# Performance work log

Hardware: AMD Instinct MI355X
Metric: run time of the kernel (lower is better)

## Reference

```python
import jax, jax.numpy as jnp
import numpy as np

B, T, S = 16, 512, 512
V, E, H = 10000, 512, 1024
L, K, MAXLEN = 6, 3, 1024
PAD_VAL = 1.0  # torch code pads conv input with tgt_pad_idx as a float value


def setup_inputs() -> dict:
    key = jax.random.key(0)
    ks = jax.random.split(key, 12)
    g = lambda k, shape: (jax.random.normal(k, shape, jnp.float32) * 0.02)
    return {
        "tgt": jax.random.randint(ks[0], (B, T), 0, V),
        "encoder_conved": jax.random.normal(ks[1], (B, S, E), jnp.float32),
        "encoder_combined": jax.random.normal(ks[2], (B, S, E), jnp.float32),
        "tok_emb": g(ks[3], (V, E)),
        "pos_emb": g(ks[4], (MAXLEN, E)),
        "emb2hid_w": g(ks[5], (E, H)), "emb2hid_b": jnp.zeros((H,), jnp.float32),
        "hid2emb_w": g(ks[6], (H, E)), "hid2emb_b": jnp.zeros((E,), jnp.float32),
        "attn_hid2emb_w": g(ks[7], (H, E)), "attn_hid2emb_b": jnp.zeros((E,), jnp.float32),
        "attn_emb2hid_w": g(ks[8], (E, H)), "attn_emb2hid_b": jnp.zeros((H,), jnp.float32),
        "fc_out_w": g(ks[9], (E, V)), "fc_out_b": jnp.zeros((V,), jnp.float32),
        "conv_w": g(ks[10], (L, 2 * H, H, K)),  # torch Conv1d weight: [out, in, k]
        "conv_b": jnp.zeros((L, 2 * H), jnp.float32),
    }


def reference(tgt, encoder_conved, encoder_combined, tok_emb, pos_emb,
              emb2hid_w, emb2hid_b, hid2emb_w, hid2emb_b,
              attn_hid2emb_w, attn_hid2emb_b, attn_emb2hid_w, attn_emb2hid_b,
              fc_out_w, fc_out_b, conv_w, conv_b):
    scale = jnp.float32(np.sqrt(0.5))
    b, t = tgt.shape
    h = emb2hid_w.shape[1]
    k = conv_w.shape[-1]

    # embeddings (dropout=0 -> identity)
    embedded = tok_emb[tgt] + pos_emb[jnp.arange(t)][None, :, :]   # [B,T,E]
    conv_input = (embedded @ emb2hid_w + emb2hid_b).transpose(0, 2, 1)  # [B,H,T]

    attention = None
    for l in range(conv_w.shape[0]):
        # causal left-pad with the (float) pad-index value, as in the torch code
        pad = jnp.full((b, h, k - 1), PAD_VAL, conv_input.dtype)
        x = jnp.concatenate([pad, conv_input], axis=2)              # [B,H,T+K-1]
        conved = jax.lax.conv_general_dilated(
            x, conv_w[l], window_strides=(1,), padding='VALID',
            dimension_numbers=('NCH', 'OIH', 'NCH')) + conv_b[l][None, :, None]  # [B,2H,T]
        a, g = jnp.split(conved, 2, axis=1)
        conved = a * jax.nn.sigmoid(g)                              # GLU -> [B,H,T]

        # single-head attention over encoder states
        conved_emb = conved.transpose(0, 2, 1) @ attn_hid2emb_w + attn_hid2emb_b  # [B,T,E]
        combined = (conved_emb + embedded) * scale
        energy = jnp.einsum('bte,bse->bts', combined, encoder_conved)
        attention = jax.nn.softmax(energy, axis=2)                  # [B,T,S]
        attended = jnp.einsum('bts,bse->bte', attention, encoder_combined)
        attended = attended @ attn_emb2hid_w + attn_emb2hid_b       # [B,T,H]
        conved = (conved + attended.transpose(0, 2, 1)) * scale     # [B,H,T]

        conv_input = (conved + conv_input) * scale                  # scaled residual

    conved = conv_input.transpose(0, 2, 1) @ hid2emb_w + hid2emb_b  # [B,T,E]
    output = conved @ fc_out_w + fc_out_b                           # [B,T,V]
    return output, attention
```

## Files before the change

### kernel.cpp

```cpp
#include <hip/hip_runtime.h>
#include <hip/hip_bf16.h>

typedef __attribute__((ext_vector_type(4))) float f32x4;
typedef __attribute__((ext_vector_type(8))) short short8;

#define DEVFN __device__ __forceinline__

static constexpr int Bn = 16, Tn = 512, Sn = 512, Vn = 10000, En = 512, Hn = 1024, Ln = 6;
static constexpr int Mn = Bn * Tn;
static constexpr float kScale = 0.70710678118654752440f;

DEVFN float bf2f(__hip_bfloat16 x) { return __bfloat162float(x); }
DEVFN __hip_bfloat16 f2bf(float x) { return __float2bfloat16(x); }

struct bf16x4 { __hip_bfloat16 x, y, z, w; };

DEVFN void gload_lds16(const short* g, short* l) {
    __builtin_amdgcn_global_load_lds((const __attribute__((address_space(1))) void*)g,
                                     (__attribute__((address_space(3))) void*)l, 16, 0, 0);
}


__global__ void padfill_kernel(__hip_bfloat16* p) {
    p[threadIdx.x] = f2bf(1.0f);
}

__global__ void embed_kernel(const int* __restrict__ tgt, const float* __restrict__ tok,
                             const float* __restrict__ pos, const float* __restrict__ bah,
                             __hip_bfloat16* __restrict__ out, __hip_bfloat16* __restrict__ outA) {
    int row = blockIdx.x;
    int t = row & (Tn - 1);
    int v = tgt[row];
    const float* tr = tok + (long)v * En;
    const float* pr = pos + (long)t * En;
    int e = threadIdx.x * 4;
    float4 a = *(const float4*)(tr + e);
    float4 b = *(const float4*)(pr + e);
    float4 bb = *(const float4*)(bah + e);
    bf16x4 o{f2bf(a.x + b.x), f2bf(a.y + b.y), f2bf(a.z + b.z), f2bf(a.w + b.w)};
    *(bf16x4*)(out + (long)row * En + e) = o;
    bf16x4 oa{f2bf(kScale * (a.x + b.x + bb.x)), f2bf(kScale * (a.y + b.y + bb.y)),
              f2bf(kScale * (a.z + b.z + bb.z)), f2bf(kScale * (a.w + b.w + bb.w))};
    *(bf16x4*)(outA + (long)row * En + e) = oa;
}

__global__ void transpose_f32_bf16(const float* __restrict__ src, __hip_bfloat16* __restrict__ dst,
                                   int R, int C, long sZi, long sZo) {
    __shared__ float tile[32][33];
    src += (long)blockIdx.z * sZi;
    dst += (long)blockIdx.z * sZo;
    int c0 = blockIdx.x * 32, r0 = blockIdx.y * 32;
    for (int i = threadIdx.y; i < 32; i += 8) {
        int r = r0 + i, c = c0 + threadIdx.x;
        tile[i][threadIdx.x] = (r < R && c < C) ? src[(long)r * C + c] : 0.f;
    }
    __syncthreads();
    for (int i = threadIdx.y; i < 32; i += 8) {
        int c = c0 + i, r = r0 + threadIdx.x;
        if (c < C && r < R) dst[(long)c * R + r] = f2bf(tile[threadIdx.x][i]);
    }
}

__global__ void convert_bf16_kernel(const float* __restrict__ src, __hip_bfloat16* __restrict__ dst, long n4) {
    long i = (long)blockIdx.x * blockDim.x + threadIdx.x;
    if (i >= n4) return;
    long j = i * 4;
    float4 v = *(const float4*)(src + j);
    bf16x4 o{f2bf(v.x), f2bf(v.y), f2bf(v.z), f2bf(v.w)};
    *(bf16x4*)(dst + j) = o;
}

__global__ void wpack_kernel(const float* __restrict__ convw, __hip_bfloat16* __restrict__ wp, int l) {
    int kk = blockIdx.x * 256 + threadIdx.x;
    int c = blockIdx.y;
    int grp = c >> 5, w = c & 31;
    int o = (w < 16) ? grp * 16 + w : Hn + grp * 16 + (w - 16);
    int i = kk & (Hn - 1);
    int tap = kk >> 10;
    long base = ((long)(l * 2 * Hn + o)) * (Hn * 3);
    wp[(long)c * (3 * Hn) + kk] = f2bf(convw[base + (long)i * 3 + tap]);
}

__global__ __launch_bounds__(256) void softmax_kernel(const float* __restrict__ energy,
                                                      float* __restrict__ attn_f32,
                                                      __hip_bfloat16* __restrict__ attn_bf) {
    int row = blockIdx.x;
    const float* e = energy + (long)row * Sn;
    int tid = threadIdx.x;
    float v0 = e[tid], v1 = e[tid + 256];
    float m = fmaxf(v0, v1);
    for (int off = 32; off; off >>= 1) m = fmaxf(m, __shfl_xor(m, off));
    __shared__ float redm[4];
    __shared__ float reds[4];
    int lane = tid & 63, w = tid >> 6;
    if (lane == 0) redm[w] = m;
    __syncthreads();
    m = fmaxf(fmaxf(redm[0], redm[1]), fmaxf(redm[2], redm[3]));
    float x0 = __expf(v0 - m), x1 = __expf(v1 - m);
    float s = x0 + x1;
    for (int off = 32; off; off >>= 1) s += __shfl_xor(s, off);
    if (lane == 0) reds[w] = s;
    __syncthreads();
    s = reds[0] + reds[1] + reds[2] + reds[3];
    float inv = 1.f / s;
    long base = (long)row * Sn;
    if (attn_f32) {
        attn_f32[base + tid] = x0 * inv;
        attn_f32[base + tid + 256] = x1 * inv;
    }
    attn_bf[base + tid] = f2bf(x0 * inv);
    attn_bf[base + tid + 256] = f2bf(x1 * inv);
}

template <int EPI, bool OUTF32, bool NBOUND>
__global__ __launch_bounds__(256) void gemm_bf16(
    const __hip_bfloat16* __restrict__ A, const __hip_bfloat16* __restrict__ Bw,
    const float* __restrict__ bias, void* __restrict__ Cout,
    const __hip_bfloat16* __restrict__ R1, const __hip_bfloat16* __restrict__ R2,
    const float* __restrict__ R1f, const __hip_bfloat16* __restrict__ padrow,
    int M, int N, int K, long aZ, long bZ, long cZ, float s1, float s2) {
    __shared__ alignas(16) short As[2][128 * 32];
    __shared__ alignas(16) short Bs[2][128 * 32];
    const int tid = threadIdx.x;
    const int lane = tid & 63;
    const int wid = tid >> 6;
    const int wr = wid >> 1, wc = wid & 1;
    const int m0 = blockIdx.y * 128, n0 = blockIdx.x * 128;
    const short* Ag = (const short*)A + (long)blockIdx.z * aZ;
    const short* Bg = (const short*)Bw + (long)blockIdx.z * bZ;
    const short* pad = (const short*)padrow;

    f32x4 acc[4][4] = {};

    const int rc = tid >> 2;
    const int k8 = (tid & 3) * 8;

    auto stage = [&](int buf, int k0) {
#pragma unroll
        for (int j = 0; j < 2; ++j) {
            int r = rc + j * 64;
            const short* asrc = Ag + (long)(m0 + r) * K + k0 + k8;
            gload_lds16(asrc, &As[buf][r * 32 + k8]);
            int n = n0 + r;
            const short* bsrc = (NBOUND && n >= N) ? (pad + k8) : (Bg + (long)n * K + k0 + k8);
            gload_lds16(bsrc, &Bs[buf][r * 32 + k8]);
        }
    };

    stage(0, 0);
    __syncthreads();

    int cur = 0;
    for (int k0 = 0; k0 < K; k0 += 32) {
        if (k0 + 32 < K) stage(cur ^ 1, k0 + 32);
        const int rsel = lane & 15, hi = (lane >> 4) * 8;
        short8 af[4], bg[4];
#pragma unroll
        for (int mi = 0; mi < 4; ++mi)
            af[mi] = *(const short8*)&As[cur][(wr * 64 + mi * 16 + rsel) * 32 + hi];
#pragma unroll
        for (int ni = 0; ni < 4; ++ni)
            bg[ni] = *(const short8*)&Bs[cur][(wc * 64 + ni * 16 + rsel) * 32 + hi];
#pragma unroll
        for (int mi = 0; mi < 4; ++mi)
#pragma unroll
            for (int ni = 0; ni < 4; ++ni)
                acc[mi][ni] = __builtin_amdgcn_mfma_f32_16x16x32_bf16(af[mi], bg[ni], acc[mi][ni], 0, 0, 0);
        __syncthreads();
        cur ^= 1;
    }

    const int rsel = lane & 15, rg = (lane >> 4) * 4;
    float* Cf = (float*)Cout + (long)blockIdx.z * cZ;
    __hip_bfloat16* Cb = (__hip_bfloat16*)Cout + (long)blockIdx.z * cZ;
    const __hip_bfloat16* R1z = R1 + (long)blockIdx.z * cZ;
    const __hip_bfloat16* R2z = R2 + (long)blockIdx.z * cZ;
    const float* R1fz = R1f + (long)blockIdx.z * cZ;
#pragma unroll
    for (int ni = 0; ni < 4; ++ni) {
        int col = n0 + wc * 64 + ni * 16 + rsel;
        if (NBOUND && col >= N) continue;
        float bi = (EPI != 3 && bias) ? bias[col] : 0.f;
#pragma unroll
        for (int mi = 0; mi < 4; ++mi) {
            int row = m0 + wr * 64 + mi * 16 + rg;
            f32x4 v = acc[mi][ni];
#pragma unroll
            for (int q = 0; q < 4; ++q) {
                long idx = (long)(row + q) * N + col;
                float x;
                if (EPI == 3) x = v[q] * s1 + R1fz[idx];
                else {
                    x = v[q] + bi;
                    if (EPI >= 1) x = (x + bf2f(R1z[idx])) * s1;
                    if (EPI >= 2) x = (x + bf2f(R2z[idx])) * s2;
                }
                if (OUTF32) Cf[idx] = x;
                else Cb[idx] = f2bf(x);
            }
        }
    }
}

template <bool OUTF32, bool GLUE, bool IM2COL, bool NBOUND>
__global__ __launch_bounds__(512, 2) void gemm256(
    const __hip_bfloat16* __restrict__ A, const __hip_bfloat16* __restrict__ Bw,
    const float* __restrict__ bias, void* __restrict__ Cout,
    const __hip_bfloat16* __restrict__ padrow, int M, int N, int K) {
    __shared__ alignas(16) short As[2][256 * 64];
    __shared__ alignas(16) short Bs[2][256 * 64];
    const int tid = threadIdx.x;
    const int lane = tid & 63;
    const int wid = tid >> 6;
    const int wr = wid >> 2, wc = wid & 3;
    const int nwg = gridDim.x * gridDim.y;
    const int orig = blockIdx.y * gridDim.x + blockIdx.x;
    const int qd = nwg >> 3, rd = nwg & 7, xc = orig & 7, loc = orig >> 3;
    const int bid = (xc < rd ? xc * (qd + 1) : rd * (qd + 1) + (xc - rd) * qd) + loc;
    const int n0 = (bid % gridDim.x) * 256, m0 = (bid / gridDim.x) * 256;
    const short* Ag = (const short*)A;
    const short* Bg = (const short*)Bw;
    const short* pad = (const short*)padrow;

    f32x4 acc[8][4] = {};

    const int srow_l = tid >> 3;
    const int scol = ((tid & 7) ^ (srow_l & 7)) * 8;
    const int sdst = (tid >> 3) * 64 + (tid & 7) * 8;

    auto stage = [&](int buf, int kt) {
        const int k0 = kt * 64;
#pragma unroll
        for (int j = 0; j < 4; ++j) {
            const int row = j * 64 + srow_l;
            const short* asrc;
            if (IM2COL) {
                int m = m0 + row;
                int t = m & (Tn - 1);
                int tap = k0 >> 10;
                int tau = t - 2 + tap;
                int kcol = (k0 & (Hn - 1)) + scol;
                asrc = (tau >= 0) ? (Ag + (long)(m - 2 + tap) * Hn + kcol) : (pad + scol);
            } else {
                asrc = Ag + (long)(m0 + row) * K + k0 + scol;
            }
            gload_lds16(asrc, &As[buf][j * 4096 + sdst]);
            int n = n0 + row;
            const short* bsrc = (NBOUND && n >= N) ? (pad + scol) : (Bg + (long)n * K + k0 + scol);
            gload_lds16(bsrc, &Bs[buf][j * 4096 + sdst]);
        }
    };

    const int rsel = lane & 15, hi = (lane >> 4) * 8;
    const int xorc = (rsel & 7) << 3;

    stage(0, 0);
    const int NT = K >> 6;
    for (int t = 0; t < NT; ++t) {
        const int cur = t & 1;
        if (t + 1 < NT) {
            stage(cur ^ 1, t + 1);
            asm volatile("s_waitcnt vmcnt(8)" ::: "memory");
        } else {
            asm volatile("s_waitcnt vmcnt(0)" ::: "memory");
        }
        __builtin_amdgcn_s_barrier();
        __builtin_amdgcn_sched_barrier(0);
        short8 bg[2][2][2];
#pragma unroll
        for (int nh = 0; nh < 2; ++nh)
#pragma unroll
            for (int i = 0; i < 2; ++i) {
                const int row = wc * 64 + nh * 32 + i * 16 + rsel;
#pragma unroll
                for (int ks = 0; ks < 2; ++ks)
                    bg[nh][i][ks] = *(const short8*)&Bs[cur][row * 64 + ((ks * 32 + hi) ^ xorc)];
            }
#pragma unroll
        for (int mh = 0; mh < 2; ++mh) {
            short8 af[4][2];
#pragma unroll
            for (int i = 0; i < 4; ++i) {
                const int row = wr * 128 + mh * 64 + i * 16 + rsel;
#pragma unroll
                for (int ks = 0; ks < 2; ++ks)
                    af[i][ks] = *(const short8*)&As[cur][row * 64 + ((ks * 32 + hi) ^ xorc)];
            }
            __builtin_amdgcn_s_setprio(1);
#pragma unroll
            for (int nh = 0; nh < 2; ++nh)
#pragma unroll
                for (int i = 0; i < 4; ++i)
#pragma unroll
                    for (int jn = 0; jn < 2; ++jn)
#pragma unroll
                        for (int ks = 0; ks < 2; ++ks)
                            acc[mh * 4 + i][nh * 2 + jn] = __builtin_amdgcn_mfma_f32_16x16x32_bf16(
                                af[i][ks], bg[nh][jn][ks], acc[mh * 4 + i][nh * 2 + jn], 0, 0, 0);
            __builtin_amdgcn_s_setprio(0);
            __builtin_amdgcn_sched_barrier(0);
        }
        __builtin_amdgcn_s_barrier();
        __builtin_amdgcn_sched_barrier(0);
    }

    const int rg = (lane >> 4) * 4;
    if (GLUE) {
        __hip_bfloat16* Cb = (__hip_bfloat16*)Cout;
        const int No = N >> 1;
#pragma unroll
        for (int p = 0; p < 2; ++p) {
            int jcol = ((n0 + wc * 64) >> 1) + p * 16 + rsel;
            float ba = bias[jcol];
            float bgv = bias[Hn + jcol];
#pragma unroll
            for (int mi = 0; mi < 8; ++mi) {
                int row = m0 + wr * 128 + mi * 16 + rg;
                f32x4 va = acc[mi][2 * p], vg = acc[mi][2 * p + 1];
#pragma unroll
                for (int q = 0; q < 4; ++q) {
                    float a = va[q] + ba;
                    float g = vg[q] + bgv;
                    Cb[(long)(row + q) * No + jcol] = f2bf(a * (1.f / (1.f + __expf(-g))));
                }
            }
        }
        return;
    }
    float* Cf = (float*)Cout;
    __hip_bfloat16* Cb = (__hip_bfloat16*)Cout;
#pragma unroll
    for (int ni = 0; ni < 4; ++ni) {
        int col = n0 + wc * 64 + ni * 16 + rsel;
        if (NBOUND && col >= N) continue;
        float bi = bias ? bias[col] : 0.f;
#pragma unroll
        for (int mi = 0; mi < 8; ++mi) {
            int row = m0 + wr * 128 + mi * 16 + rg;
            f32x4 v = acc[mi][ni];
#pragma unroll
            for (int q = 0; q < 4; ++q) {
                long idx = (long)(row + q) * N + col;
                float x = v[q] + bi;
                if (OUTF32) Cf[idx] = x;
                else Cb[idx] = f2bf(x);
            }
        }
    }
}


extern "C" void kernel_launch(void* const* d_in, const int* in_sizes, int n_in,
                              void* d_out, int out_size, void* d_ws, size_t ws_size,
                              hipStream_t stream) {
    const int* tgt = (const int*)d_in[0];
    const float* enc_conved = (const float*)d_in[1];
    const float* enc_combined = (const float*)d_in[2];
    const float* tok_emb = (const float*)d_in[3];
    const float* pos_emb = (const float*)d_in[4];
    const float* w_e2h = (const float*)d_in[5];
    const float* b_e2h = (const float*)d_in[6];
    const float* w_h2e = (const float*)d_in[7];
    const float* b_h2e = (const float*)d_in[8];
    const float* w_ah2e = (const float*)d_in[9];
    const float* b_ah2e = (const float*)d_in[10];
    const float* w_ae2h = (const float*)d_in[11];
    const float* b_ae2h = (const float*)d_in[12];
    const float* w_fc = (const float*)d_in[13];
    const float* b_fc = (const float*)d_in[14];
    const float* conv_w = (const float*)d_in[15];
    const float* conv_b = (const float*)d_in[16];

    char* ws = (char*)d_ws;
    size_t off = 0;
    auto alloc = [&](size_t bytes) { size_t r = off; off = (off + bytes + 255) & ~(size_t)255; return r; };
    __hip_bfloat16* emb    = (__hip_bfloat16*)(ws + alloc((size_t)Mn * En * 2));
    __hip_bfloat16* embA   = (__hip_bfloat16*)(ws + alloc((size_t)Mn * En * 2));
    __hip_bfloat16* convin = (__hip_bfloat16*)(ws + alloc((size_t)Mn * Hn * 2));
    __hip_bfloat16* conved = (__hip_bfloat16*)(ws + alloc((size_t)Mn * Hn * 2));
    size_t o_en = alloc((size_t)Mn * Sn * 4);
    float* energy = (float*)(ws + o_en);
    __hip_bfloat16* encm = (__hip_bfloat16*)(ws + o_en);
    __hip_bfloat16* attnbf = (__hip_bfloat16*)(ws + alloc((size_t)Mn * Sn * 2));
    __hip_bfloat16* wT_e2h = (__hip_bfloat16*)(ws + alloc((size_t)Hn * En * 2));
    __hip_bfloat16* wT_h2e = (__hip_bfloat16*)(ws + alloc((size_t)En * Hn * 2));
    __hip_bfloat16* wT_ae2h= (__hip_bfloat16*)(ws + alloc((size_t)Hn * En * 2));
    __hip_bfloat16* wbAH   = (__hip_bfloat16*)(ws + alloc((size_t)Hn * En * 2));
    __hip_bfloat16* wT_fc  = (__hip_bfloat16*)(ws + alloc((size_t)Vn * En * 2));
    __hip_bfloat16* wpack  = (__hip_bfloat16*)(ws + alloc((size_t)2 * Hn * 3 * Hn * 2));
    __hip_bfloat16* encc   = (__hip_bfloat16*)(ws + alloc((size_t)Bn * Sn * En * 2));
    __hip_bfloat16* encAH  = (__hip_bfloat16*)(ws + alloc((size_t)Bn * Sn * Hn * 2));
    __hip_bfloat16* encCW  = (__hip_bfloat16*)(ws + alloc((size_t)Bn * Hn * Sn * 2));
    float* embE            = (float*)(ws + alloc((size_t)Mn * Sn * 4));
    __hip_bfloat16* padrow = (__hip_bfloat16*)(ws + alloc(256));
    __hip_bfloat16* tmpE   = conved;

    float* out = (float*)d_out;
    float* attn_out = out + (long)Mn * Vn;
    const long bSq = (long)Sn * Sn;
    const long bSH = (long)Sn * Hn;

    dim3 tb(32, 8);
    const __hip_bfloat16* nb = nullptr;
    const float* nf = nullptr;

    padfill_kernel<<<1, 128, 0, stream>>>(padrow);
    embed_kernel<<<Mn, 128, 0, stream>>>(tgt, tok_emb, pos_emb, b_ah2e, emb, embA);
    transpose_f32_bf16<<<dim3(Hn / 32, En / 32, 1), tb, 0, stream>>>(w_e2h, wT_e2h, En, Hn, 0, 0);
    transpose_f32_bf16<<<dim3(En / 32, Hn / 32, 1), tb, 0, stream>>>(w_h2e, wT_h2e, Hn, En, 0, 0);
    transpose_f32_bf16<<<dim3(Hn / 32, En / 32, 1), tb, 0, stream>>>(w_ae2h, wT_ae2h, En, Hn, 0, 0);
    transpose_f32_bf16<<<dim3((Vn + 31) / 32, En / 32, 1), tb, 0, stream>>>(w_fc, wT_fc, En, Vn, 0, 0);
    convert_bf16_kernel<<<((long)Hn * En / 4 + 255) / 256, 256, 0, stream>>>(w_ah2e, wbAH, (long)Hn * En / 4);
    convert_bf16_kernel<<<((long)Bn * Sn * En / 4 + 255) / 256, 256, 0, stream>>>(enc_conved, encc, (long)Bn * Sn * En / 4);
    convert_bf16_kernel<<<((long)Bn * Sn * En / 4 + 255) / 256, 256, 0, stream>>>(enc_combined, encm, (long)Bn * Sn * En / 4);

    gemm_bf16<0, false, false><<<dim3(Hn / 128, Sn / 128, Bn), 256, 0, stream>>>(
        encc, wbAH, nullptr, encAH, nb, nb, nf, padrow, Sn, Hn, En, bSq, 0, bSH, 1.f, 1.f);
    gemm_bf16<0, false, false><<<dim3(Sn / 128, Hn / 128, Bn), 256, 0, stream>>>(
        wT_ae2h, encm, nullptr, encCW, nb, nb, nf, padrow, Hn, Sn, En, 0, bSq, bSH, 1.f, 1.f);
    gemm_bf16<0, true, false><<<dim3(Sn / 128, Tn / 128, Bn), 256, 0, stream>>>(
        embA, encc, nullptr, embE, nb, nb, nf, padrow, Tn, Sn, En, bSq, bSq, bSq, 1.f, 1.f);
    gemm_bf16<0, false, false><<<dim3(Hn / 128, Mn / 128, 1), 256, 0, stream>>>(
        emb, wT_e2h, b_e2h, convin, nb, nb, nf, padrow, Mn, Hn, En, 0, 0, 0, 1.f, 1.f);

    for (int l = 0; l < Ln; ++l) {
        wpack_kernel<<<dim3(3 * Hn / 256, 2 * Hn, 1), 256, 0, stream>>>(conv_w, wpack, l);
        gemm256<false, true, true, false><<<dim3(2 * Hn / 256, Mn / 256, 1), 512, 0, stream>>>(
            convin, wpack, conv_b + (long)l * 2 * Hn, conved, padrow, Mn, 2 * Hn, 3 * Hn);
        gemm_bf16<3, true, false><<<dim3(Sn / 128, Tn / 128, Bn), 256, 0, stream>>>(
            conved, encAH, nullptr, energy, nb, nb, embE, padrow,
            Tn, Sn, Hn, (long)Tn * Hn, bSH, bSq, kScale, 1.f);
        softmax_kernel<<<Mn, 256, 0, stream>>>(energy, (l == Ln - 1) ? attn_out : nullptr, attnbf);
        gemm_bf16<2, false, false><<<dim3(Hn / 128, Tn / 128, Bn), 256, 0, stream>>>(
            attnbf, encCW, b_ae2h, convin, conved, convin, nf, padrow,
            Tn, Hn, Sn, bSq, bSH, (long)Tn * Hn, kScale, kScale);
    }

    gemm_bf16<0, false, false><<<dim3(En / 128, Mn / 128, 1), 256, 0, stream>>>(
        convin, wT_h2e, b_h2e, tmpE, nb, nb, nf, padrow, Mn, En, Hn, 0, 0, 0, 1.f, 1.f);
    gemm256<true, false, false, true><<<dim3((Vn + 255) / 256, Mn / 256, 1), 512, 0, stream>>>(
        tmpE, wT_fc, b_fc, out, padrow, Mn, Vn, En);
}
```

Baseline: 1.375 ms.

## Fuse energy GEMM, embedding-energy term and softmax into one attention kernel

Replaces the per-layer energy GEMM (fp32 energy output plus a precomputed fp32 embedding-energy residual) and the separate softmax kernel with one fused kernel. It computes a 128x512 row tile per block by chaining the K loops over conved·encAH and embA·encc, with the scale folded into the attn_hid2emb weights, then does the row softmax in registers and writes bf16 and, on the last layer, fp32. This removes the fp32 energy round trip and the embE buffer. Separately, all six layers' conv weights are packed once up front when workspace allows, instead of once per layer. The risks are the low block count (64 blocks) and the higher register pressure of the 4x8 accumulator.

```diff
diff --git a/kernel.cpp b/kernel.cpp
--- a/kernel.cpp
+++ b/kernel.cpp
@@ -61,55 +61,165 @@
     }
 }
 
-__global__ void convert_bf16_kernel(const float* __restrict__ src, __hip_bfloat16* __restrict__ dst, long n4) {
+__global__ void convert_bf16_kernel(const float* __restrict__ src, __hip_bfloat16* __restrict__ dst,
+                                    long n4, float sc) {
     long i = (long)blockIdx.x * blockDim.x + threadIdx.x;
     if (i >= n4) return;
     long j = i * 4;
     float4 v = *(const float4*)(src + j);
-    bf16x4 o{f2bf(v.x), f2bf(v.y), f2bf(v.z), f2bf(v.w)};
+    bf16x4 o{f2bf(v.x * sc), f2bf(v.y * sc), f2bf(v.z * sc), f2bf(v.w * sc)};
     *(bf16x4*)(dst + j) = o;
 }
 
-__global__ void wpack_kernel(const float* __restrict__ convw, __hip_bfloat16* __restrict__ wp, int l) {
+__global__ void wpack_kernel(const float* __restrict__ convw, __hip_bfloat16* __restrict__ wp,
+                             int lbase, long zstride) {
     int kk = blockIdx.x * 256 + threadIdx.x;
     int c = blockIdx.y;
+    int l = lbase + blockIdx.z;
     int grp = c >> 5, w = c & 31;
     int o = (w < 16) ? grp * 16 + w : Hn + grp * 16 + (w - 16);
     int i = kk & (Hn - 1);
     int tap = kk >> 10;
     long base = ((long)(l * 2 * Hn + o)) * (Hn * 3);
-    wp[(long)c * (3 * Hn) + kk] = f2bf(convw[base + (long)i * 3 + tap]);
-}
-
-__global__ __launch_bounds__(256) void softmax_kernel(const float* __restrict__ energy,
-                                                      float* __restrict__ attn_f32,
-                                                      __hip_bfloat16* __restrict__ attn_bf) {
-    int row = blockIdx.x;
-    const float* e = energy + (long)row * Sn;
-    int tid = threadIdx.x;
-    float v0 = e[tid], v1 = e[tid + 256];
-    float m = fmaxf(v0, v1);
-    for (int off = 32; off; off >>= 1) m = fmaxf(m, __shfl_xor(m, off));
-    __shared__ float redm[4];
-    __shared__ float reds[4];
-    int lane = tid & 63, w = tid >> 6;
-    if (lane == 0) redm[w] = m;
+    wp[(long)blockIdx.z * zstride + (long)c * (3 * Hn) + kk] = f2bf(convw[base + (long)i * 3 + tap]);
+}
+
+template <bool LAST>
+__global__ __launch_bounds__(512) void attn_fused(
+    const __hip_bfloat16* __restrict__ conved, const __hip_bfloat16* __restrict__ encAHs,
+    const __hip_bfloat16* __restrict__ embA, const __hip_bfloat16* __restrict__ encc,
+    __hip_bfloat16* __restrict__ attn_bf, float* __restrict__ attn_f32) {
+    __shared__ alignas(16) short Asl[2][128 * 32];
+    __shared__ alignas(16) short Bsl[2][512 * 32];
+    __shared__ float redm[2][64][4];
+    __shared__ float reds[2][64][4];
+    const int tid = threadIdx.x;
+    const int lane = tid & 63;
+    const int wid = tid >> 6;
+    const int wr = wid >> 2, wc = wid & 3;
+    const int m0 = blockIdx.x * 128;
+    const int z = blockIdx.y;
+    const long grow0 = (long)z * Tn + m0;
+    const short* A1 = (const short*)conved + grow0 * Hn;
+    const short* B1 = (const short*)encAHs + (long)z * Sn * Hn;
+    const short* A2 = (const short*)embA + grow0 * En;
+    const short* B2 = (const short*)encc + (long)z * Sn * En;
+    constexpr int NT1 = Hn / 32, NT2 = En / 32, NT = NT1 + NT2;
+
+    f32x4 acc[4][8] = {};
+
+    const int sr = tid >> 2;
+    const int sc = (tid & 3) * 8;
+
+    auto stage = [&](int buf, int t) {
+        const short *Ag, *Bg; int stA, k0;
+        if (t < NT1) { Ag = A1; Bg = B1; stA = Hn; k0 = t * 32; }
+        else         { Ag = A2; Bg = B2; stA = En; k0 = (t - NT1) * 32; }
+        gload_lds16(Ag + (long)sr * stA + k0 + sc, &Asl[buf][sr * 32 + sc]);
+#pragma unroll
+        for (int j = 0; j < 4; ++j) {
+            int rb = j * 128 + sr;
+            gload_lds16(Bg + (long)rb * stA + k0 + sc, &Bsl[buf][rb * 32 + sc]);
+        }
+    };
+
+    const int rsel = lane & 15, hi8 = (lane >> 4) * 8;
+
+    stage(0, 0);
+    for (int t = 0; t < NT; ++t) {
+        const int cur = t & 1;
+        if (t + 1 < NT) {
+            stage(cur ^ 1, t + 1);
+            asm volatile("s_waitcnt vmcnt(5)" ::: "memory");
+        } else {
+            asm volatile("s_waitcnt vmcnt(0)" ::: "memory");
+        }
+        __builtin_amdgcn_s_barrier();
+        __builtin_amdgcn_sched_barrier(0);
+        short8 af[4], bgv[8];
+#pragma unroll
+        for (int mi = 0; mi < 4; ++mi)
+            af[mi] = *(const short8*)&Asl[cur][(wr * 64 + mi * 16 + rsel) * 32 + hi8];
+#pragma unroll
+        for (int ni = 0; ni < 8; ++ni)
+            bgv[ni] = *(const short8*)&Bsl[cur][(wc * 128 + ni * 16 + rsel) * 32 + hi8];
+        __builtin_amdgcn_s_setprio(1);
+#pragma unroll
+        for (int mi = 0; mi < 4; ++mi)
+#pragma unroll
+            for (int ni = 0; ni < 8; ++ni)
+                acc[mi][ni] = __builtin_amdgcn_mfma_f32_16x16x32_bf16(af[mi], bgv[ni], acc[mi][ni], 0, 0, 0);
+        __builtin_amdgcn_s_setprio(0);
+        __builtin_amdgcn_s_barrier();
+        __builtin_amdgcn_sched_barrier(0);
+    }
+
+    const int h = lane >> 4;
+    float Mx[4][4];
+#pragma unroll
+    for (int mi = 0; mi < 4; ++mi)
+#pragma unroll
+        for (int q = 0; q < 4; ++q) {
+            float m = acc[mi][0][q];
+#pragma unroll
+            for (int ni = 1; ni < 8; ++ni) m = fmaxf(m, acc[mi][ni][q]);
+            m = fmaxf(m, __shfl_xor(m, 1));
+            m = fmaxf(m, __shfl_xor(m, 2));
+            m = fmaxf(m, __shfl_xor(m, 4));
+            m = fmaxf(m, __shfl_xor(m, 8));
+            Mx[mi][q] = m;
+        }
+    if (rsel == 0) {
+#pragma unroll
+        for (int mi = 0; mi < 4; ++mi)
+#pragma unroll
+            for (int q = 0; q < 4; ++q)
+                redm[wr][mi * 16 + h * 4 + q][wc] = Mx[mi][q];
+    }
     __syncthreads();
-    m = fmaxf(fmaxf(redm[0], redm[1]), fmaxf(redm[2], redm[3]));
-    float x0 = __expf(v0 - m), x1 = __expf(v1 - m);
-    float s = x0 + x1;
-    for (int off = 32; off; off >>= 1) s += __shfl_xor(s, off);
-    if (lane == 0) reds[w] = s;
+    float Sv[4][4];
+#pragma unroll
+    for (int mi = 0; mi < 4; ++mi)
+#pragma unroll
+        for (int q = 0; q < 4; ++q) {
+            const float* rm = redm[wr][mi * 16 + h * 4 + q];
+            float m = fmaxf(fmaxf(rm[0], rm[1]), fmaxf(rm[2], rm[3]));
+            float s = 0.f;
+#pragma unroll
+            for (int ni = 0; ni < 8; ++ni) {
+                float e = __expf(acc[mi][ni][q] - m);
+                acc[mi][ni][q] = e;
+                s += e;
+            }
+            s += __shfl_xor(s, 1);
+            s += __shfl_xor(s, 2);
+            s += __shfl_xor(s, 4);
+            s += __shfl_xor(s, 8);
+            Sv[mi][q] = s;
+        }
+    if (rsel == 0) {
+#pragma unroll
+        for (int mi = 0; mi < 4; ++mi)
+#pragma unroll
+            for (int q = 0; q < 4; ++q)
+                reds[wr][mi * 16 + h * 4 + q][wc] = Sv[mi][q];
+    }
     __syncthreads();
-    s = reds[0] + reds[1] + reds[2] + reds[3];
-    float inv = 1.f / s;
-    long base = (long)row * Sn;
-    if (attn_f32) {
-        attn_f32[base + tid] = x0 * inv;
-        attn_f32[base + tid + 256] = x1 * inv;
-    }
-    attn_bf[base + tid] = f2bf(x0 * inv);
-    attn_bf[base + tid + 256] = f2bf(x1 * inv);
+#pragma unroll
+    for (int mi = 0; mi < 4; ++mi)
+#pragma unroll
+        for (int q = 0; q < 4; ++q) {
+            const float* rs = reds[wr][mi * 16 + h * 4 + q];
+            float inv = 1.f / (rs[0] + rs[1] + rs[2] + rs[3]);
+            long gr = grow0 + wr * 64 + mi * 16 + h * 4 + q;
+#pragma unroll
+            for (int ni = 0; ni < 8; ++ni) {
+                int col = wc * 128 + ni * 16 + rsel;
+                float v = acc[mi][ni][q] * inv;
+                attn_bf[gr * Sn + col] = f2bf(v);
+                if (LAST) attn_f32[gr * Sn + col] = v;
+            }
+        }
 }
 
 template <int EPI, bool OUTF32, bool NBOUND>
@@ -117,7 +227,7 @@
     const __hip_bfloat16* __restrict__ A, const __hip_bfloat16* __restrict__ Bw,
     const float* __restrict__ bias, void* __restrict__ Cout,
     const __hip_bfloat16* __restrict__ R1, const __hip_bfloat16* __restrict__ R2,
-    const float* __restrict__ R1f, const __hip_bfloat16* __restrict__ padrow,
+    const __hip_bfloat16* __restrict__ padrow,
     int M, int N, int K, long aZ, long bZ, long cZ, float s1, float s2) {
     __shared__ alignas(16) short As[2][128 * 32];
     __shared__ alignas(16) short Bs[2][128 * 32];
@@ -175,12 +285,11 @@
     __hip_bfloat16* Cb = (__hip_bfloat16*)Cout + (long)blockIdx.z * cZ;
     const __hip_bfloat16* R1z = R1 + (long)blockIdx.z * cZ;
     const __hip_bfloat16* R2z = R2 + (long)blockIdx.z * cZ;
-    const float* R1fz = R1f + (long)blockIdx.z * cZ;
 #pragma unroll
     for (int ni = 0; ni < 4; ++ni) {
         int col = n0 + wc * 64 + ni * 16 + rsel;
         if (NBOUND && col >= N) continue;
-        float bi = (EPI != 3 && bias) ? bias[col] : 0.f;
+        float bi = bias ? bias[col] : 0.f;
 #pragma unroll
         for (int mi = 0; mi < 4; ++mi) {
             int row = m0 + wr * 64 + mi * 16 + rg;
@@ -188,13 +297,9 @@
 #pragma unroll
             for (int q = 0; q < 4; ++q) {
                 long idx = (long)(row + q) * N + col;
-                float x;
-                if (EPI == 3) x = v[q] * s1 + R1fz[idx];
-                else {
-                    x = v[q] + bi;
-                    if (EPI >= 1) x = (x + bf2f(R1z[idx])) * s1;
-                    if (EPI >= 2) x = (x + bf2f(R2z[idx])) * s2;
-                }
+                float x = v[q] + bi;
+                if (EPI >= 1) x = (x + bf2f(R1z[idx])) * s1;
+                if (EPI >= 2) x = (x + bf2f(R2z[idx])) * s2;
                 if (OUTF32) Cf[idx] = x;
                 else Cb[idx] = f2bf(x);
             }
@@ -378,22 +483,21 @@
     __hip_bfloat16* embA   = (__hip_bfloat16*)(ws + alloc((size_t)Mn * En * 2));
     __hip_bfloat16* convin = (__hip_bfloat16*)(ws + alloc((size_t)Mn * Hn * 2));
     __hip_bfloat16* conved = (__hip_bfloat16*)(ws + alloc((size_t)Mn * Hn * 2));
-    size_t o_en = alloc((size_t)Mn * Sn * 4);
-    float* energy = (float*)(ws + o_en);
-    __hip_bfloat16* encm = (__hip_bfloat16*)(ws + o_en);
     __hip_bfloat16* attnbf = (__hip_bfloat16*)(ws + alloc((size_t)Mn * Sn * 2));
+    __hip_bfloat16* encm   = (__hip_bfloat16*)(ws + alloc((size_t)Bn * Sn * En * 2));
     __hip_bfloat16* wT_e2h = (__hip_bfloat16*)(ws + alloc((size_t)Hn * En * 2));
     __hip_bfloat16* wT_h2e = (__hip_bfloat16*)(ws + alloc((size_t)En * Hn * 2));
     __hip_bfloat16* wT_ae2h= (__hip_bfloat16*)(ws + alloc((size_t)Hn * En * 2));
-    __hip_bfloat16* wbAH   = (__hip_bfloat16*)(ws + alloc((size_t)Hn * En * 2));
+    __hip_bfloat16* wbAHs  = (__hip_bfloat16*)(ws + alloc((size_t)Hn * En * 2));
     __hip_bfloat16* wT_fc  = (__hip_bfloat16*)(ws + alloc((size_t)Vn * En * 2));
-    __hip_bfloat16* wpack  = (__hip_bfloat16*)(ws + alloc((size_t)2 * Hn * 3 * Hn * 2));
     __hip_bfloat16* encc   = (__hip_bfloat16*)(ws + alloc((size_t)Bn * Sn * En * 2));
-    __hip_bfloat16* encAH  = (__hip_bfloat16*)(ws + alloc((size_t)Bn * Sn * Hn * 2));
+    __hip_bfloat16* encAHs = (__hip_bfloat16*)(ws + alloc((size_t)Bn * Sn * Hn * 2));
     __hip_bfloat16* encCW  = (__hip_bfloat16*)(ws + alloc((size_t)Bn * Hn * Sn * 2));
-    float* embE            = (float*)(ws + alloc((size_t)Mn * Sn * 4));
     __hip_bfloat16* padrow = (__hip_bfloat16*)(ws + alloc(256));
-    __hip_bfloat16* tmpE   = conved;
+    const size_t W1 = (size_t)2 * Hn * 3 * Hn * 2;
+    bool packAll = (off + 6 * W1 + 256 <= ws_size);
+    __hip_bfloat16* wpack = (__hip_bfloat16*)(ws + alloc(packAll ? 6 * W1 : W1));
+    __hip_bfloat16* tmpE = conved;
 
     float* out = (float*)d_out;
     float* attn_out = out + (long)Mn * Vn;
@@ -402,7 +506,6 @@
 
     dim3 tb(32, 8);
     const __hip_bfloat16* nb = nullptr;
-    const float* nf = nullptr;
 
     padfill_kernel<<<1, 128, 0, stream>>>(padrow);
     embed_kernel<<<Mn, 128, 0, stream>>>(tgt, tok_emb, pos_emb, b_ah2e, emb, embA);
@@ -410,34 +513,36 @@
     transpose_f32_bf16<<<dim3(En / 32, Hn / 32, 1), tb, 0, stream>>>(w_h2e, wT_h2e, Hn, En, 0, 0);
     transpose_f32_bf16<<<dim3(Hn / 32, En / 32, 1), tb, 0, stream>>>(w_ae2h, wT_ae2h, En, Hn, 0, 0);
     transpose_f32_bf16<<<dim3((Vn + 31) / 32, En / 32, 1), tb, 0, stream>>>(w_fc, wT_fc, En, Vn, 0, 0);
-    convert_bf16_kernel<<<((long)Hn * En / 4 + 255) / 256, 256, 0, stream>>>(w_ah2e, wbAH, (long)Hn * En / 4);
-    convert_bf16_kernel<<<((long)Bn * Sn * En / 4 + 255) / 256, 256, 0, stream>>>(enc_conved, encc, (long)Bn * Sn * En / 4);
-    convert_bf16_kernel<<<((long)Bn * Sn * En / 4 + 255) / 256, 256, 0, stream>>>(enc_combined, encm, (long)Bn * Sn * En / 4);
+    convert_bf16_kernel<<<((long)Hn * En / 4 + 255) / 256, 256, 0, stream>>>(w_ah2e, wbAHs, (long)Hn * En / 4, kScale);
+    convert_bf16_kernel<<<((long)Bn * Sn * En / 4 + 255) / 256, 256, 0, stream>>>(enc_conved, encc, (long)Bn * Sn * En / 4, 1.f);
+    convert_bf16_kernel<<<((long)Bn * Sn * En / 4 + 255) / 256, 256, 0, stream>>>(enc_combined, encm, (long)Bn * Sn * En / 4, 1.f);
+    if (packAll)
+        wpack_kernel<<<dim3(3 * Hn / 256, 2 * Hn, Ln), 256, 0, stream>>>(conv_w, wpack, 0, (long)2 * Hn * 3 * Hn);
 
     gemm_bf16<0, false, false><<<dim3(Hn / 128, Sn / 128, Bn), 256, 0, stream>>>(
-        encc, wbAH, nullptr, encAH, nb, nb, nf, padrow, Sn, Hn, En, bSq, 0, bSH, 1.f, 1.f);
+        encc, wbAHs, nullptr, encAHs, nb, nb, padrow, Sn, Hn, En, bSq, 0, bSH, 1.f, 1.f);
     gemm_bf16<0, false, false><<<dim3(Sn / 128, Hn / 128, Bn), 256, 0, stream>>>(
-        wT_ae2h, encm, nullptr, encCW, nb, nb, nf, padrow, Hn, Sn, En, 0, bSq, bSH, 1.f, 1.f);
-    gemm_bf16<0, true, false><<<dim3(Sn / 128, Tn / 128, Bn), 256, 0, stream>>>(
-        embA, encc, nullptr, embE, nb, nb, nf, padrow, Tn, Sn, En, bSq, bSq, bSq, 1.f, 1.f);
+        wT_ae2h, encm, nullptr, encCW, nb, nb, padrow, Hn, Sn, En, 0, bSq, bSH, 1.f, 1.f);
     gemm_bf16<0, false, false><<<dim3(Hn / 128, Mn / 128, 1), 256, 0, stream>>>(
-        emb, wT_e2h, b_e2h, convin, nb, nb, nf, padrow, Mn, Hn, En, 0, 0, 0, 1.f, 1.f);
+        emb, wT_e2h, b_e2h, convin, nb, nb, padrow, Mn, Hn, En, 0, 0, 0, 1.f, 1.f);
 
     for (int l = 0; l < Ln; ++l) {
-        wpack_kernel<<<dim3(3 * Hn / 256, 2 * Hn, 1), 256, 0, stream>>>(conv_w, wpack, l);
+        __hip_bfloat16* wpl = wpack + (packAll ? (size_t)l * (2 * Hn) * (3 * Hn) : 0);
+        if (!packAll)
+            wpack_kernel<<<dim3(3 * Hn / 256, 2 * Hn, 1), 256, 0, stream>>>(conv_w, wpack, l, 0);
         gemm256<false, true, true, false><<<dim3(2 * Hn / 256, Mn / 256, 1), 512, 0, stream>>>(
-            convin, wpack, conv_b + (long)l * 2 * Hn, conved, padrow, Mn, 2 * Hn, 3 * Hn);
-        gemm_bf16<3, true, false><<<dim3(Sn / 128, Tn / 128, Bn), 256, 0, stream>>>(
-            conved, encAH, nullptr, energy, nb, nb, embE, padrow,
-            Tn, Sn, Hn, (long)Tn * Hn, bSH, bSq, kScale, 1.f);
-        softmax_kernel<<<Mn, 256, 0, stream>>>(energy, (l == Ln - 1) ? attn_out : nullptr, attnbf);
+            convin, wpl, conv_b + (long)l * 2 * Hn, conved, padrow, Mn, 2 * Hn, 3 * Hn);
+        if (l == Ln - 1)
+            attn_fused<true><<<dim3(Tn / 128, Bn), 512, 0, stream>>>(conved, encAHs, embA, encc, attnbf, attn_out);
+        else
+            attn_fused<false><<<dim3(Tn / 128, Bn), 512, 0, stream>>>(conved, encAHs, embA, encc, attnbf, nullptr);
         gemm_bf16<2, false, false><<<dim3(Hn / 128, Tn / 128, Bn), 256, 0, stream>>>(
-            attnbf, encCW, b_ae2h, convin, conved, convin, nf, padrow,
+            attnbf, encCW, b_ae2h, convin, conved, convin, padrow,
             Tn, Hn, Sn, bSq, bSH, (long)Tn * Hn, kScale, kScale);
     }
 
     gemm_bf16<0, false, false><<<dim3(En / 128, Mn / 128, 1), 256, 0, stream>>>(
-        convin, wT_h2e, b_h2e, tmpE, nb, nb, nf, padrow, Mn, En, Hn, 0, 0, 0, 1.f, 1.f);
+        convin, wT_h2e, b_h2e, tmpE, nb, nb, padrow, Mn, En, Hn, 0, 0, 0, 1.f, 1.f);
     gemm256<true, false, false, true><<<dim3((Vn + 255) / 256, Mn / 256, 1), 512, 0, stream>>>(
         tmpE, wT_fc, b_fc, out, padrow, Mn, Vn, En);
 }
```

After: 1.668 ms. 21.3% more time.
